# Optimization experiments

Hardware: AMD Instinct MI355X
Metric: run time of the kernel (lower is better)

The kernel has to match this reference:

```python
import jax, jax.numpy as jnp
import numpy as np

N = 10000    # nodes in batched graph
E = 160000   # edges (avg degree 16)
G = 64       # graphs in batch
F_IN = 128
H = 256      # hidden width (forced equal everywhere by fc_1(1024,..) and readout sums)
HEADS = 2


def setup_inputs() -> dict:
    ks = jax.random.split(jax.random.key(0), 24)
    def w(k, shape, fan_in):
        return jax.random.normal(k, shape, dtype=jnp.float32) * np.float32(1.0 / np.sqrt(fan_in))
    return {
        "h": jax.random.normal(ks[0], (N, F_IN), dtype=jnp.float32),
        "src": jax.random.randint(ks[1], (E,), 0, N, dtype=jnp.int32),
        "dst": jax.random.randint(ks[2], (E,), 0, N, dtype=jnp.int32),
        # sorted graph ids, every graph guaranteed non-empty (avoids -inf from MaxPooling)
        "graph_ids": ((jnp.arange(N) * G) // N).astype(jnp.int32),
        "gcn1_W": w(ks[3], (F_IN, H), F_IN), "gcn1_b": jnp.zeros((H,), jnp.float32),
        "gcn2_W": w(ks[4], (H, H), H),       "gcn2_b": jnp.zeros((H,), jnp.float32),
        "gcn3_W": w(ks[5], (H, H), H),       "gcn3_b": jnp.zeros((H,), jnp.float32),
        "gat1_W": w(ks[6], (F_IN, HEADS * H), F_IN),
        "gat1_al": w(ks[7], (HEADS, H), H), "gat1_ar": w(ks[8], (HEADS, H), H),
        "gat1_b": jnp.zeros((HEADS * H,), jnp.float32),
        "gat2_W": w(ks[9], (H, HEADS * H), H),
        "gat2_al": w(ks[10], (HEADS, H), H), "gat2_ar": w(ks[11], (HEADS, H), H),
        "gat2_b": jnp.zeros((HEADS * H,), jnp.float32),
        "gat3_W": w(ks[12], (H, HEADS * H), H),
        "gat3_al": w(ks[13], (HEADS, H), H), "gat3_ar": w(ks[14], (HEADS, H), H),
        "gat3_b": jnp.zeros((HEADS * H,), jnp.float32),
        "fc1_W": w(ks[15], (4 * H, 128), 4 * H), "fc1_b": jnp.zeros((128,), jnp.float32),
        "fc2_W": w(ks[16], (128, 2), 128),       "fc2_b": jnp.zeros((2,), jnp.float32),
    }


def _forward(h, src, dst, graph_ids,
             gcn1_W, gcn1_b, gcn2_W, gcn2_b, gcn3_W, gcn3_b,
             gat1_W, gat1_al, gat1_ar, gat1_b,
             gat2_W, gat2_al, gat2_ar, gat2_b,
             gat3_W, gat3_al, gat3_ar, gat3_b,
             fc1_W, fc1_b, fc2_W, fc2_b):
    ones_e = jnp.ones((E,), jnp.float32)
    # DGL GraphConv norm='both': D_out^{-1/2} on src side, D_in^{-1/2} on dst side (deg clamped to 1)
    d_src = jnp.clip(jax.ops.segment_sum(ones_e, src, num_segments=N), 1.0) ** -0.5
    d_dst = jnp.clip(jax.ops.segment_sum(ones_e, dst, num_segments=N), 1.0) ** -0.5
    counts = jnp.clip(jax.ops.segment_sum(jnp.ones((N,), jnp.float32), graph_ids, num_segments=G), 1.0)

    def gcn(x, W, b):
        agg = jax.ops.segment_sum((x * d_src[:, None])[src], dst, num_segments=N) * d_dst[:, None]
        return jax.nn.relu(agg @ W + b)

    def gat(x, W, al, ar, b):
        z = (x @ W).reshape(N, HEADS, H)                 # [N, heads, H]
        e = jax.nn.leaky_relu(jnp.sum(z * al, -1)[src] + jnp.sum(z * ar, -1)[dst], 0.2)  # [E, heads]
        ex = jnp.exp(e - jax.ops.segment_max(e, dst, num_segments=N)[dst])
        alpha = ex / jax.ops.segment_sum(ex, dst, num_segments=N)[dst]  # edge softmax per dst
        o = jax.ops.segment_sum(alpha[:, :, None] * z[src], dst, num_segments=N)  # [N, heads, H]
        return jax.nn.relu(o + b.reshape(1, HEADS, H)).mean(axis=1)     # mean over heads, as in source

    def avgp(x):
        return jax.ops.segment_sum(x, graph_ids, num_segments=G) / counts[:, None]
    def maxp(x):
        return jax.ops.segment_max(x, graph_ids, num_segments=G)
    def readout(x):
        return jnp.concatenate([avgp(x), maxp(x)], axis=1)

    gcn1 = gcn(h, gcn1_W, gcn1_b);   r1 = readout(gcn1)
    gcn2 = gcn(gcn1, gcn2_W, gcn2_b); r2 = readout(gcn2)
    gcn3 = gcn(gcn2, gcn3_W, gcn3_b); r3 = readout(gcn3)
    g1 = gat(h, gat1_W, gat1_al, gat1_ar, gat1_b)   # spat_read_out1 computed but unused (faithful)
    g2 = gat(g1, gat2_W, gat2_al, gat2_ar, gat2_b); s2 = readout(g2)
    g3 = gat(g2, gat3_W, gat3_al, gat3_ar, gat3_b)
    s3 = jnp.concatenate([avgp(g2), maxp(g3)], axis=1)  # source: avg(gat2), max(gat3)

    spec = r1 + r2 + r3
    spat = r1 + s2 + s3  # source bug preserved: spat_merged starts from spec_read_out1
    merged = jnp.concatenate([spec, spat], axis=1)       # [G, 1024]
    f1 = jax.nn.relu(merged @ fc1_W + fc1_b)             # dropout p=0.0 -> identity
    return jax.nn.sigmoid(f1 @ fc2_W + fc2_b)            # [G, 2]


def reference(h, src, dst, graph_ids,
              gcn1_W, gcn1_b, gcn2_W, gcn2_b, gcn3_W, gcn3_b,
              gat1_W, gat1_al, gat1_ar, gat1_b,
              gat2_W, gat2_al, gat2_ar, gat2_b,
              gat3_W, gat3_al, gat3_ar, gat3_b,
              fc1_W, fc1_b, fc2_W, fc2_b):
    return _forward(h, src, dst, graph_ids,
                    gcn1_W, gcn1_b, gcn2_W, gcn2_b, gcn3_W, gcn3_b,
                    gat1_W, gat1_al, gat1_ar, gat1_b,
                    gat2_W, gat2_al, gat2_ar, gat2_b,
                    gat3_W, gat3_al, gat3_ar, gat3_b,
                    fc1_W, fc1_b, fc2_W, fc2_b)
```

## Files before the change

kernel.cpp:

```cpp
#include <hip/hip_runtime.h>
#include <math.h>

#define NN 10000
#define EE 160000
#define GG 64
#define FIN 128
#define HH 256
#define ZW 512
#define RS 8
#define MAXDEG 128

typedef unsigned short u16;
using bf16x8 = __attribute__((ext_vector_type(8))) short;
using f32x4 = __attribute__((ext_vector_type(4))) float;

__device__ inline u16 f2bf(float x) {
  union { float f; unsigned u; } v; v.f = x;
  unsigned r = v.u + 0x7FFF + ((v.u >> 16) & 1);
  return (u16)(r >> 16);
}
__device__ inline float bf2f(u16 x) {
  union { unsigned u; float f; } v; v.u = ((unsigned)x) << 16; return v.f;
}
__device__ inline float bflo(unsigned pair) {
  union { unsigned u; float f; } v; v.u = pair << 16; return v.f;
}
__device__ inline float bfhi(unsigned pair) {
  union { unsigned u; float f; } v; v.u = pair & 0xFFFF0000u; return v.f;
}

#define BM 128
#define BN 64
#define BK 64
#define LPAD 8

struct SmemGemm { u16 As[BM][BK + LPAD]; u16 Bs[BN][BK + LPAD]; };
struct SmemGatGemm { u16 A[2][64][BK + LPAD]; u16 B[2][64][BK + LPAD]; };
struct SmemFuseV2 {
  float al[4][2][MAXDEG];
  int   idx[4][MAXDEG];
  float inv[4][2];
  float mm[4][2];
};


__global__ __launch_bounds__(256) void k_count_prep(
    const int* __restrict__ src, const int* __restrict__ dst, int* deg_src, int* deg_dst,
    const float* __restrict__ gcn1_W, u16* __restrict__ gcn1_Wt,
    const float* __restrict__ gcn2_W, u16* __restrict__ gcn2_Wt,
    const float* __restrict__ gcn3_W, u16* __restrict__ gcn3_Wt,
    const float* __restrict__ gat1_W, u16* __restrict__ gat1_Wt,
    const float* __restrict__ gat2_W, u16* __restrict__ gat2_Wt,
    const float* __restrict__ gat3_W, u16* __restrict__ gat3_Wt,
    const float* __restrict__ h, u16* __restrict__ h_bf,
    const float* __restrict__ al1, const float* __restrict__ ar1,
    const float* __restrict__ al2, const float* __restrict__ ar2,
    const float* __restrict__ al3, const float* __restrict__ ar3,
    float* __restrict__ wl1, float* __restrict__ wr1,
    float* __restrict__ wl2, float* __restrict__ wr2,
    float* __restrict__ wl3, float* __restrict__ wr3) {
  int bb = blockIdx.x, t = threadIdx.x;
  if (bb < 625) {
    int e = bb * 256 + t;
    if (e < EE) {
      atomicAdd(&deg_src[src[e]], 1);
      atomicAdd(&deg_dst[dst[e]], 1);
    }
    return;
  }
  int b = bb - 625;
  if (b < 1920) {
    const float* W; u16* Wt; int K, N, idx;
    if (b < 128)       { W = gcn1_W; Wt = gcn1_Wt; K = 128; N = 256; idx = b * 256 + t; }
    else if (b < 384)  { W = gcn2_W; Wt = gcn2_Wt; K = 256; N = 256; idx = (b - 128) * 256 + t; }
    else if (b < 640)  { W = gcn3_W; Wt = gcn3_Wt; K = 256; N = 256; idx = (b - 384) * 256 + t; }
    else if (b < 896)  { W = gat1_W; Wt = gat1_Wt; K = 128; N = 512; idx = (b - 640) * 256 + t; }
    else if (b < 1408) { W = gat2_W; Wt = gat2_Wt; K = 256; N = 512; idx = (b - 896) * 256 + t; }
    else               { W = gat3_W; Wt = gat3_Wt; K = 256; N = 512; idx = (b - 1408) * 256 + t; }
    int k = idx / N, n = idx - k * N;
    Wt[(size_t)n * K + k] = f2bf(W[idx]);
  } else if (b < 3170) {
    int idx = (b - 1920) * 256 + t;
    float4 v = *(const float4*)&h[(size_t)idx * 4];
    ushort4 o;
    o.x = f2bf(v.x); o.y = f2bf(v.y); o.z = f2bf(v.z); o.w = f2bf(v.w);
    *(ushort4*)&h_bf[(size_t)idx * 4] = o;
  } else {
    int jb = b - 3170;
    const float* W; const float* al; const float* ar; float* wl; float* wr; int K, i;
    if (jb == 0)      { W = gat1_W; al = al1; ar = ar1; wl = wl1; wr = wr1; K = 128; i = t; }
    else if (jb <= 2) { W = gat2_W; al = al2; ar = ar2; wl = wl2; wr = wr2; K = 256; i = (jb - 1) * 256 + t; }
    else              { W = gat3_W; al = al3; ar = ar3; wl = wl3; wr = wr3; K = 256; i = (jb - 3) * 256 + t; }
    int hh = i / K, k = i - hh * K;
    float sl = 0.f, sr = 0.f;
    for (int f = 0; f < HH; f++) {
      float wv = W[(size_t)k * ZW + hh * HH + f];
      sl += wv * al[hh * HH + f];
      sr += wv * ar[hh * HH + f];
    }
    wl[hh * K + k] = sl;
    wr[hh * K + k] = sr;
  }
}

__global__ __launch_bounds__(1024) void k_norms_scan(
    const int* __restrict__ deg_src, const int* __restrict__ deg_dst,
    const int* __restrict__ gid, float* dsrc, float* ddst, int* gstart, int* row_ptr) {
  if (blockIdx.x < 10) {
    int n = blockIdx.x * 1024 + threadIdx.x;
    if (n < NN) {
      int a = deg_src[n]; if (a < 1) a = 1;
      int b = deg_dst[n]; if (b < 1) b = 1;
      dsrc[n] = 1.0f / sqrtf((float)a);
      ddst[n] = 1.0f / sqrtf((float)b);
      if (n == 0) gstart[gid[0]] = 0;
      else if (gid[n] != gid[n - 1]) gstart[gid[n]] = n;
      if (n == NN - 1) gstart[GG] = NN;
    }
    return;
  }
  __shared__ int wsum[16];
  __shared__ int carry;
  int lane = threadIdx.x & 63, wid = threadIdx.x >> 6;
  if (threadIdx.x == 0) { carry = 0; row_ptr[0] = 0; }
  __syncthreads();
  for (int base = 0; base < NN; base += 1024) {
    int i = base + threadIdx.x;
    int x = (i < NN) ? deg_dst[i] : 0;
#pragma unroll
    for (int off = 1; off < 64; off <<= 1) {
      int t = __shfl_up(x, off);
      if (lane >= off) x += t;
    }
    if (lane == 63) wsum[wid] = x;
    __syncthreads();
    if (wid == 0 && lane < 16) {
      int y = wsum[lane];
#pragma unroll
      for (int off = 1; off < 16; off <<= 1) {
        int t = __shfl_up(y, off, 16);
        if (lane >= off) y += t;
      }
      wsum[lane] = y;
    }
    __syncthreads();
    int woff = (wid > 0) ? wsum[wid - 1] : 0;
    if (i < NN) row_ptr[i + 1] = carry + woff + x;
    int total = wsum[15];
    __syncthreads();
    if (threadIdx.x == 0) carry += total;
    __syncthreads();
  }
}

__global__ __launch_bounds__(64) void sort_rows_kernel(const int* __restrict__ row_ptr,
                                                       int* csr_src) {
  int n = blockIdx.x;
  int s0 = row_ptr[n];
  int L = row_ptr[n + 1] - s0;
  if (L <= 1) return;
  __shared__ int buf[512];
  if (L <= 512) {
    for (int i = threadIdx.x; i < L; i += 64) buf[i] = csr_src[s0 + i];
    __syncthreads();
    for (int i = threadIdx.x; i < L; i += 64) {
      int v = buf[i], r = 0;
      for (int j = 0; j < L; j++) {
        int u = buf[j];
        r += (u < v) || (u == v && j < i);
      }
      csr_src[s0 + r] = v;
    }
  } else if (threadIdx.x == 0) {
    for (int i = s0 + 1; i < s0 + L; i++) {
      int v = csr_src[i], j = i - 1;
      while (j >= s0 && csr_src[j] > v) { csr_src[j + 1] = csr_src[j]; j--; }
      csr_src[j + 1] = v;
    }
  }
}


__device__ inline void dev_gcn_agg(int n, int lane,
    const u16* __restrict__ xb, const float* __restrict__ dsrc, const float* __restrict__ ddst,
    const int* __restrict__ row_ptr, const int* __restrict__ csr_src,
    u16* __restrict__ out, int F) {
  int s0 = row_ptr[n], s1 = row_ptr[n + 1];
  float dd = ddst[n];
  if (F == 256) {
    int bf = lane * 4;
    float a0 = 0, a1 = 0, a2 = 0, a3 = 0;
    int e = s0;
    for (; e + 1 < s1; e += 2) {
      int sA = csr_src[e], sB = csr_src[e + 1];
      float wA = dsrc[sA], wB = dsrc[sB];
      uint2 vA = *(const uint2*)&xb[(size_t)sA * 256 + bf];
      uint2 vB = *(const uint2*)&xb[(size_t)sB * 256 + bf];
      a0 += wA * bflo(vA.x) + wB * bflo(vB.x);
      a1 += wA * bfhi(vA.x) + wB * bfhi(vB.x);
      a2 += wA * bflo(vA.y) + wB * bflo(vB.y);
      a3 += wA * bfhi(vA.y) + wB * bfhi(vB.y);
    }
    if (e < s1) {
      int s = csr_src[e];
      float w = dsrc[s];
      uint2 v = *(const uint2*)&xb[(size_t)s * 256 + bf];
      a0 += w * bflo(v.x); a1 += w * bfhi(v.x);
      a2 += w * bflo(v.y); a3 += w * bfhi(v.y);
    }
    ushort4 o;
    o.x = f2bf(a0 * dd); o.y = f2bf(a1 * dd); o.z = f2bf(a2 * dd); o.w = f2bf(a3 * dd);
    *(ushort4*)&out[(size_t)n * 256 + bf] = o;
  } else {
    int bf = lane * 2;
    float a0 = 0, a1 = 0;
    int e = s0;
    for (; e + 1 < s1; e += 2) {
      int sA = csr_src[e], sB = csr_src[e + 1];
      float wA = dsrc[sA], wB = dsrc[sB];
      unsigned vA = *(const unsigned*)&xb[(size_t)sA * 128 + bf];
      unsigned vB = *(const unsigned*)&xb[(size_t)sB * 128 + bf];
      a0 += wA * bflo(vA) + wB * bflo(vB);
      a1 += wA * bfhi(vA) + wB * bfhi(vB);
    }
    if (e < s1) {
      int s = csr_src[e];
      float w = dsrc[s];
      unsigned v = *(const unsigned*)&xb[(size_t)s * 128 + bf];
      a0 += w * bflo(v); a1 += w * bfhi(v);
    }
    ushort2 o;
    o.x = f2bf(a0 * dd); o.y = f2bf(a1 * dd);
    *(ushort2*)&out[(size_t)n * 128 + bf] = o;
  }
}

__device__ inline void dev_scores(int n, int lane, const float* __restrict__ x,
                                  const float* __restrict__ wl, const float* __restrict__ wr,
                                  float* __restrict__ asrc, float* __restrict__ adst, int K) {
  float a0 = 0, a1 = 0, b0 = 0, b1 = 0;
  for (int k = lane; k < K; k += 64) {
    float xv = x[(size_t)n * K + k];
    a0 += xv * wl[k];
    a1 += xv * wl[K + k];
    b0 += xv * wr[k];
    b1 += xv * wr[K + k];
  }
#pragma unroll
  for (int off = 32; off; off >>= 1) {
    a0 += __shfl_down(a0, off);
    a1 += __shfl_down(a1, off);
    b0 += __shfl_down(b0, off);
    b1 += __shfl_down(b1, off);
  }
  if (lane == 0) {
    asrc[n * 2 + 0] = a0; asrc[n * 2 + 1] = a1;
    adst[n * 2 + 0] = b0; adst[n * 2 + 1] = b1;
  }
}

__device__ inline void dev_scores_bf(int n, int lane, const u16* __restrict__ xb,
                                     const float* __restrict__ wl, const float* __restrict__ wr,
                                     float* __restrict__ asrc, float* __restrict__ adst) {
  float a0 = 0, a1 = 0, b0 = 0, b1 = 0;
#pragma unroll
  for (int idx = lane; idx < 128; idx += 64) {
    unsigned v = *(const unsigned*)&xb[(size_t)n * 256 + idx * 2];
    float lo = bflo(v), hi = bfhi(v);
    a0 += lo * wl[idx * 2] + hi * wl[idx * 2 + 1];
    a1 += lo * wl[256 + idx * 2] + hi * wl[256 + idx * 2 + 1];
    b0 += lo * wr[idx * 2] + hi * wr[idx * 2 + 1];
    b1 += lo * wr[256 + idx * 2] + hi * wr[256 + idx * 2 + 1];
  }
#pragma unroll
  for (int off = 32; off; off >>= 1) {
    a0 += __shfl_down(a0, off);
    a1 += __shfl_down(a1, off);
    b0 += __shfl_down(b0, off);
    b1 += __shfl_down(b1, off);
  }
  if (lane == 0) {
    asrc[n * 2 + 0] = a0; asrc[n * 2 + 1] = a1;
    adst[n * 2 + 0] = b0; adst[n * 2 + 1] = b1;
  }
}

template<int F>
__device__ inline void dev_gatfuse_v3(int n0, int tid,
    const u16* __restrict__ xb,
    const float* __restrict__ asrc, const float* __restrict__ adst,
    const int* __restrict__ row_ptr, const int* __restrict__ csr_src,
    u16* __restrict__ gx, SmemFuseV2& sf) {
  int w = tid >> 6, lane = tid & 63;
  {
    int n = n0 + w;
    int s0 = row_ptr[n];
    int deg = row_ptr[n + 1] - s0;
    float2 an = *(const float2*)&adst[n * 2];
    float m0 = -INFINITY, m1 = -INFINITY;
    if (deg <= MAXDEG) {
      for (int i = lane; i < deg; i += 64) {
        int s = csr_src[s0 + i];
        sf.idx[w][i] = s;
        float2 as = *(const float2*)&asrc[s * 2];
        float e0 = as.x + an.x; e0 = (e0 > 0.f) ? e0 : 0.2f * e0;
        float e1 = as.y + an.y; e1 = (e1 > 0.f) ? e1 : 0.2f * e1;
        sf.al[w][0][i] = e0; sf.al[w][1][i] = e1;
        m0 = fmaxf(m0, e0); m1 = fmaxf(m1, e1);
      }
#pragma unroll
      for (int off = 32; off; off >>= 1) {
        m0 = fmaxf(m0, __shfl_xor(m0, off));
        m1 = fmaxf(m1, __shfl_xor(m1, off));
      }
      float t0 = 0.f, t1 = 0.f;
      for (int i = lane; i < deg; i += 64) {
        float w0 = __expf(sf.al[w][0][i] - m0);
        float w1 = __expf(sf.al[w][1][i] - m1);
        sf.al[w][0][i] = w0; sf.al[w][1][i] = w1;
        t0 += w0; t1 += w1;
      }
#pragma unroll
      for (int off = 32; off; off >>= 1) {
        t0 += __shfl_xor(t0, off);
        t1 += __shfl_xor(t1, off);
      }
      if (lane == 0) {
        sf.inv[w][0] = (t0 > 0.f) ? 1.f / t0 : 0.f;
        sf.inv[w][1] = (t1 > 0.f) ? 1.f / t1 : 0.f;
      }
    } else {
      for (int i = lane; i < deg; i += 64) {
        float2 as = *(const float2*)&asrc[csr_src[s0 + i] * 2];
        float e0 = as.x + an.x; e0 = (e0 > 0.f) ? e0 : 0.2f * e0;
        float e1 = as.y + an.y; e1 = (e1 > 0.f) ? e1 : 0.2f * e1;
        m0 = fmaxf(m0, e0); m1 = fmaxf(m1, e1);
      }
#pragma unroll
      for (int off = 32; off; off >>= 1) {
        m0 = fmaxf(m0, __shfl_xor(m0, off));
        m1 = fmaxf(m1, __shfl_xor(m1, off));
      }
      float t0 = 0.f, t1 = 0.f;
      for (int i = lane; i < deg; i += 64) {
        float2 as = *(const float2*)&asrc[csr_src[s0 + i] * 2];
        float e0 = as.x + an.x; e0 = (e0 > 0.f) ? e0 : 0.2f * e0;
        float e1 = as.y + an.y; e1 = (e1 > 0.f) ? e1 : 0.2f * e1;
        t0 += __expf(e0 - m0); t1 += __expf(e1 - m1);
      }
#pragma unroll
      for (int off = 32; off; off >>= 1) {
        t0 += __shfl_xor(t0, off);
        t1 += __shfl_xor(t1, off);
      }
      if (lane == 0) {
        sf.inv[w][0] = (t0 > 0.f) ? 1.f / t0 : 0.f;
        sf.inv[w][1] = (t1 > 0.f) ? 1.f / t1 : 0.f;
        sf.mm[w][0] = m0; sf.mm[w][1] = m1;
      }
    }
  }
  __syncthreads();
  int slot = w;
  int p = lane;
  int n = n0 + slot;
  int s0 = row_ptr[n];
  int deg = row_ptr[n + 1] - s0;
  float i0 = sf.inv[slot][0], i1 = sf.inv[slot][1];
  if (F == 256) {
    float a0[4] = {0, 0, 0, 0}, a1[4] = {0, 0, 0, 0};
    if (deg <= MAXDEG) {
      int i = 0;
      for (; i + 1 < deg; i += 2) {
        int sA = sf.idx[slot][i], sB = sf.idx[slot][i + 1];
        float wA0 = sf.al[slot][0][i] * i0, wA1 = sf.al[slot][1][i] * i1;
        float wB0 = sf.al[slot][0][i + 1] * i0, wB1 = sf.al[slot][1][i + 1] * i1;
        uint2 vA = *(const uint2*)&xb[(size_t)sA * 256 + p * 4];
        uint2 vB = *(const uint2*)&xb[(size_t)sB * 256 + p * 4];
        float fA[4] = {bflo(vA.x), bfhi(vA.x), bflo(vA.y), bfhi(vA.y)};
        float fB[4] = {bflo(vB.x), bfhi(vB.x), bflo(vB.y), bfhi(vB.y)};
#pragma unroll
        for (int j = 0; j < 4; j++) {
          a0[j] += wA0 * fA[j] + wB0 * fB[j];
          a1[j] += wA1 * fA[j] + wB1 * fB[j];
        }
      }
      if (i < deg) {
        int s = sf.idx[slot][i];
        float w0 = sf.al[slot][0][i] * i0, w1 = sf.al[slot][1][i] * i1;
        uint2 v = *(const uint2*)&xb[(size_t)s * 256 + p * 4];
        float fv[4] = {bflo(v.x), bfhi(v.x), bflo(v.y), bfhi(v.y)};
#pragma unroll
        for (int j = 0; j < 4; j++) {
          a0[j] += w0 * fv[j];
          a1[j] += w1 * fv[j];
        }
      }
    } else {
      float mh0 = sf.mm[slot][0], mh1 = sf.mm[slot][1];
      float2 an = *(const float2*)&adst[n * 2];
      for (int i = 0; i < deg; i++) {
        int s = csr_src[s0 + i];
        float2 as = *(const float2*)&asrc[s * 2];
        float e0 = as.x + an.x; e0 = (e0 > 0.f) ? e0 : 0.2f * e0;
        float e1 = as.y + an.y; e1 = (e1 > 0.f) ? e1 : 0.2f * e1;
        float w0 = __expf(e0 - mh0) * i0, w1 = __expf(e1 - mh1) * i1;
        uint2 v = *(const uint2*)&xb[(size_t)s * 256 + p * 4];
        float fv[4] = {bflo(v.x), bfhi(v.x), bflo(v.y), bfhi(v.y)};
#pragma unroll
        for (int j = 0; j < 4; j++) {
          a0[j] += w0 * fv[j];
          a1[j] += w1 * fv[j];
        }
      }
    }
    ushort4 o0, o1;
    o0.x = f2bf(a0[0]); o0.y = f2bf(a0[1]); o0.z = f2bf(a0[2]); o0.w = f2bf(a0[3]);
    o1.x = f2bf(a1[0]); o1.y = f2bf(a1[1]); o1.z = f2bf(a1[2]); o1.w = f2bf(a1[3]);
    *(ushort4*)&gx[(size_t)n * 512 + p * 4] = o0;
    *(ushort4*)&gx[(size_t)n * 512 + 256 + p * 4] = o1;
  } else {
    float a00 = 0.f, a01 = 0.f, a10 = 0.f, a11 = 0.f;
    if (deg <= MAXDEG) {
      int i = 0;
      for (; i + 1 < deg; i += 2) {
        int sA = sf.idx[slot][i], sB = sf.idx[slot][i + 1];
        float wA0 = sf.al[slot][0][i] * i0, wA1 = sf.al[slot][1][i] * i1;
        float wB0 = sf.al[slot][0][i + 1] * i0, wB1 = sf.al[slot][1][i + 1] * i1;
        unsigned vA = *(const unsigned*)&xb[(size_t)sA * 128 + p * 2];
        unsigned vB = *(const unsigned*)&xb[(size_t)sB * 128 + p * 2];
        float lA = bflo(vA), hA = bfhi(vA), lB = bflo(vB), hB = bfhi(vB);
        a00 += wA0 * lA + wB0 * lB; a01 += wA0 * hA + wB0 * hB;
        a10 += wA1 * lA + wB1 * lB; a11 += wA1 * hA + wB1 * hB;
      }
      if (i < deg) {
        int s = sf.idx[slot][i];
        float w0 = sf.al[slot][0][i] * i0, w1 = sf.al[slot][1][i] * i1;
        unsigned v = *(const unsigned*)&xb[(size_t)s * 128 + p * 2];
        float lo = bflo(v), hi = bfhi(v);
        a00 += w0 * lo; a01 += w0 * hi;
        a10 += w1 * lo; a11 += w1 * hi;
      }
    } else {
      float mh0 = sf.mm[slot][0], mh1 = sf.mm[slot][1];
      float2 an = *(const float2*)&adst[n * 2];
      for (int i = 0; i < deg; i++) {
        int s = csr_src[s0 + i];
        float2 as = *(const float2*)&asrc[s * 2];
        float e0 = as.x + an.x; e0 = (e0 > 0.f) ? e0 : 0.2f * e0;
        float e1 = as.y + an.y; e1 = (e1 > 0.f) ? e1 : 0.2f * e1;
        float w0 = __expf(e0 - mh0) * i0, w1 = __expf(e1 - mh1) * i1;
        unsigned v = *(const unsigned*)&xb[(size_t)s * 128 + p * 2];
        float lo = bflo(v), hi = bfhi(v);
        a00 += w0 * lo; a01 += w0 * hi;
        a10 += w1 * lo; a11 += w1 * hi;
      }
    }
    ushort2 o0; o0.x = f2bf(a00); o0.y = f2bf(a01);
    ushort2 o1; o1.x = f2bf(a10); o1.y = f2bf(a11);
    *(ushort2*)&gx[(size_t)n * 256 + p * 2] = o0;
    *(ushort2*)&gx[(size_t)n * 256 + 128 + p * 2] = o1;
  }
}

__device__ inline void dev_gemm(const u16* __restrict__ A, const u16* __restrict__ Wt,
                                const float* __restrict__ bias, u16* __restrict__ Cb,
                                int K, int Nc, int relu, int bx, int by, int tid,
                                SmemGemm& sm) {
  int lane = tid & 63;
  int wid = tid >> 6;
  int wm = wid & 1, wn = wid >> 1;
  int l15 = lane & 15, lg = lane >> 4;
  int row0 = bx * BM;
  int col0 = by * BN;
  f32x4 acc[4][2] = {};
  for (int k0 = 0; k0 < K; k0 += BK) {
#pragma unroll
    for (int p = 0; p < 4; p++) {
      int c = p * 256 + tid;
      int r = c >> 3, k8 = c & 7;
      uint4 v = make_uint4(0, 0, 0, 0);
      int gr = row0 + r;
      if (gr < NN) v = *(const uint4*)&A[(size_t)gr * K + k0 + k8 * 8];
      *(uint4*)&sm.As[r][k8 * 8] = v;
    }
#pragma unroll
    for (int p = 0; p < 2; p++) {
      int c = p * 256 + tid;
      int r = c >> 3, k8 = c & 7;
      uint4 v = *(const uint4*)&Wt[(size_t)(col0 + r) * K + k0 + k8 * 8];
      *(uint4*)&sm.Bs[r][k8 * 8] = v;
    }
    __syncthreads();
#pragma unroll
    for (int ks = 0; ks < BK; ks += 32) {
      bf16x8 afr[4], bfr[2];
#pragma unroll
      for (int m = 0; m < 4; m++)
        afr[m] = *(const bf16x8*)&sm.As[wm * 64 + m * 16 + l15][ks + lg * 8];
#pragma unroll
      for (int nn = 0; nn < 2; nn++)
        bfr[nn] = *(const bf16x8*)&sm.Bs[wn * 32 + nn * 16 + l15][ks + lg * 8];
#pragma unroll
      for (int m = 0; m < 4; m++)
#pragma unroll
        for (int nn = 0; nn < 2; nn++)
          acc[m][nn] = __builtin_amdgcn_mfma_f32_16x16x32_bf16(afr[m], bfr[nn], acc[m][nn], 0, 0, 0);
    }
    __syncthreads();
  }
#pragma unroll
  for (int m = 0; m < 4; m++) {
#pragma unroll
    for (int nn = 0; nn < 2; nn++) {
      int gc = col0 + wn * 32 + nn * 16 + l15;
      float bv = bias ? bias[gc] : 0.f;
#pragma unroll
      for (int j = 0; j < 4; j++) {
        int gr = row0 + wm * 64 + m * 16 + lg * 4 + j;
        if (gr < NN) {
          float v = acc[m][nn][j] + bv;
          if (relu) v = fmaxf(v, 0.f);
          Cb[(size_t)gr * Nc + gc] = f2bf(v);
        }
      }
    }
  }
}

__device__ inline void dev_gat_gemm(const u16* __restrict__ gx, const u16* __restrict__ Wt,
                                    const float* __restrict__ bias, u16* __restrict__ gb,
                                    int K, int bx, int by, int tid, SmemGatGemm& sm) {
  int lane = tid & 63;
  int wid = tid >> 6;
  int wm = wid & 1, wn = wid >> 1;
  int l15 = lane & 15, lg = lane >> 4;
  int row0 = bx * 64;
  int col0 = by * 64;
  int str = 2 * K;
  f32x4 acc[2][2][2] = {};
  for (int k0 = 0; k0 < K; k0 += BK) {
#pragma unroll
    for (int hh = 0; hh < 2; hh++) {
#pragma unroll
      for (int p = 0; p < 2; p++) {
        int c = p * 256 + tid;
        int r = c >> 3, k8 = c & 7;
        int gr = row0 + r;
        uint4 v = make_uint4(0, 0, 0, 0);
        if (gr < NN) v = *(const uint4*)&gx[(size_t)gr * str + hh * K + k0 + k8 * 8];
        *(uint4*)&sm.A[hh][r][k8 * 8] = v;
      }
#pragma unroll
      for (int p = 0; p < 2; p++) {
        int c = p * 256 + tid;
        int r = c >> 3, k8 = c & 7;
        uint4 v = *(const uint4*)&Wt[(size_t)(hh * 256 + col0 + r) * K + k0 + k8 * 8];
        *(uint4*)&sm.B[hh][r][k8 * 8] = v;
      }
    }
    __syncthreads();
#pragma unroll
    for (int ks = 0; ks < BK; ks += 32) {
      bf16x8 af[2][2], bf_[2][2];
#pragma unroll
      for (int hh = 0; hh < 2; hh++) {
#pragma unroll
        for (int m = 0; m < 2; m++)
          af[hh][m] = *(const bf16x8*)&sm.A[hh][wm * 32 + m * 16 + l15][ks + lg * 8];
#pragma unroll
        for (int nn = 0; nn < 2; nn++)
          bf_[hh][nn] = *(const bf16x8*)&sm.B[hh][wn * 32 + nn * 16 + l15][ks + lg * 8];
      }
#pragma unroll
      for (int hh = 0; hh < 2; hh++)
#pragma unroll
        for (int m = 0; m < 2; m++)
#pragma unroll
          for (int nn = 0; nn < 2; nn++)
            acc[hh][m][nn] = __builtin_amdgcn_mfma_f32_16x16x32_bf16(af[hh][m], bf_[hh][nn], acc[hh][m][nn], 0, 0, 0);
    }
    __syncthreads();
  }
#pragma unroll
  for (int m = 0; m < 2; m++) {
#pragma unroll
    for (int nn = 0; nn < 2; nn++) {
      int gc = col0 + wn * 32 + nn * 16 + l15;
      float bv0 = bias[gc], bv1 = bias[256 + gc];
#pragma unroll
      for (int j = 0; j < 4; j++) {
        int gr = row0 + wm * 32 + m * 16 + lg * 4 + j;
        if (gr < NN) {
          float r0 = fmaxf(acc[0][m][nn][j] + bv0, 0.f);
          float r1 = fmaxf(acc[1][m][nn][j] + bv1, 0.f);
          gb[(size_t)gr * 256 + gc] = f2bf(0.5f * (r0 + r1));
        }
      }
    }
  }
}

__device__ inline void dev_stage1(const u16* __restrict__ x, int l, int g, int s, int f,
                                  const int* __restrict__ gstart, float* __restrict__ partial) {
  int n0 = gstart[g], n1 = gstart[g + 1];
  int cnt = n1 - n0;
  int chunk = (cnt + RS - 1) / RS;
  int a = n0 + s * chunk;
  int bnd = a + chunk; if (bnd > n1) bnd = n1;
  float sum = 0.f, mx = -INFINITY;
  for (int n = a; n < bnd; n++) {
    float v = bf2f(x[(size_t)n * HH + f]);
    sum += v;
    mx = fmaxf(mx, v);
  }
  size_t base = ((size_t)l * GG * RS + g * RS + s) * 2 * HH;
  partial[base + f] = sum;
  partial[base + HH + f] = mx;
}

__device__ inline float dev_stage2_val(const float* __restrict__ partial, int l, int g, int tt,
                                       const int* __restrict__ gstart) {
  int f = tt & 255, ismax = tt >> 8;
  size_t base = ((size_t)l * GG * RS + g * RS) * 2 * HH;
  if (!ismax) {
    float s = 0.f;
    for (int k = 0; k < RS; k++) s += partial[base + (size_t)k * 2 * HH + f];
    return s / (float)(gstart[g + 1] - gstart[g]);
  } else {
    float m = -INFINITY;
    for (int k = 0; k < RS; k++) m = fmaxf(m, partial[base + (size_t)k * 2 * HH + HH + f]);
    return m;
  }
}


__global__ __launch_bounds__(256) void k_fill_scores(
    const int* __restrict__ src, const int* __restrict__ dst,
    const int* __restrict__ row_ptr, int* fill, int* csr_src,
    const float* __restrict__ h, const float* __restrict__ wl1, const float* __restrict__ wr1,
    float* __restrict__ asrc, float* __restrict__ adst) {
  int b = blockIdx.x, t = threadIdx.x;
  if (b < 625) {
    int e = b * 256 + t;
    if (e < EE) {
      int d = dst[e];
      int p = atomicAdd(&fill[d], 1);
      csr_src[row_ptr[d] + p] = src[e];
    }
  } else {
    int n = (b - 625) * 4 + (t >> 6);
    if (n < NN) dev_scores(n, t & 63, h, wl1, wr1, asrc, adst, FIN);
  }
}

__global__ __launch_bounds__(256) void k_a1(
    const u16* __restrict__ h_bf, const float* __restrict__ dsrc, const float* __restrict__ ddst,
    const int* __restrict__ row_ptr, const int* __restrict__ csr_src,
    u16* __restrict__ zagg, const float* __restrict__ asrc, const float* __restrict__ adst,
    u16* __restrict__ gx) {
  __shared__ SmemFuseV2 sf;
  int b = blockIdx.x, t = threadIdx.x;
  if (b < 2500) {
    int n = b * 4 + (t >> 6);
    dev_gcn_agg(n, t & 63, h_bf, dsrc, ddst, row_ptr, csr_src, zagg, FIN);
  } else {
    dev_gatfuse_v3<128>((b - 2500) * 4, t, h_bf, asrc, adst, row_ptr, csr_src, gx, sf);
  }
}

__global__ __launch_bounds__(256) void k_b(
    const u16* __restrict__ zagg, const u16* __restrict__ gcn_Wt, const float* __restrict__ gcn_b,
    u16* __restrict__ ab_out, int Kg,
    const u16* __restrict__ gx, const u16* __restrict__ gat_Wt, const float* __restrict__ gat_b,
    u16* __restrict__ gb_out, int Ka) {
  __shared__ union { SmemGemm g; SmemGatGemm gg; } sm;
  int b = blockIdx.x, t = threadIdx.x;
  if (b < 316) {
    dev_gemm(zagg, gcn_Wt, gcn_b, ab_out, Kg, HH, 1, b % 79, b / 79, t, sm.g);
  } else {
    int i = b - 316;
    dev_gat_gemm(gx, gat_Wt, gat_b, gb_out, Ka, i / 4, i % 4, t, sm.gg);
  }
}

__global__ __launch_bounds__(256) void k_sc(
    const u16* __restrict__ gb_prev, const float* __restrict__ wl, const float* __restrict__ wr,
    float* __restrict__ asrc, float* __restrict__ adst) {
  int n = blockIdx.x * 4 + (threadIdx.x >> 6);
  dev_scores_bf(n, threadIdx.x & 63, gb_prev, wl, wr, asrc, adst);
}

__global__ __launch_bounds__(256) void k_af(
    const u16* __restrict__ ab_prev, const float* __restrict__ dsrc, const float* __restrict__ ddst,
    const int* __restrict__ row_ptr, const int* __restrict__ csr_src, u16* __restrict__ zagg,
    const u16* __restrict__ gb_prev, const float* __restrict__ asrc, const float* __restrict__ adst,
    u16* __restrict__ gx) {
  __shared__ SmemFuseV2 sf;
  int b = blockIdx.x, t = threadIdx.x;
  if (b < 2500) {
    int n = b * 4 + (t >> 6);
    dev_gcn_agg(n, t & 63, ab_prev, dsrc, ddst, row_ptr, csr_src, zagg, HH);
  } else {
    dev_gatfuse_v3<256>((b - 2500) * 4, t, gb_prev, asrc, adst, row_ptr, csr_src, gx, sf);
  }
}

struct Acts3 { const u16* a[3]; };
__global__ __launch_bounds__(256) void k_af3(
    const u16* __restrict__ ab_prev, const float* __restrict__ dsrc, const float* __restrict__ ddst,
    const int* __restrict__ row_ptr, const int* __restrict__ csr_src, u16* __restrict__ zagg,
    const u16* __restrict__ gb_prev, const float* __restrict__ asrc, const float* __restrict__ adst,
    u16* __restrict__ gx,
    Acts3 acts, const int* __restrict__ gstart, float* __restrict__ partial) {
  __shared__ SmemFuseV2 sf;
  int b = blockIdx.x, t = threadIdx.x;
  if (b < 2500) {
    int n = b * 4 + (t >> 6);
    dev_gcn_agg(n, t & 63, ab_prev, dsrc, ddst, row_ptr, csr_src, zagg, HH);
  } else if (b < 5000) {
    dev_gatfuse_v3<256>((b - 2500) * 4, t, gb_prev, asrc, adst, row_ptr, csr_src, gx, sf);
  } else {
    int i = b - 5000;
    int li = i >> 9, rem = i & 511;
    int lmap[3] = {0, 1, 3};
    dev_stage1(acts.a[li], lmap[li], rem >> 3, rem & 7, t, gstart, partial);
  }
}

__global__ __launch_bounds__(256) void k_r(
    const u16* __restrict__ ab3, const u16* __restrict__ gb3,
    const int* __restrict__ gstart, float* __restrict__ partial) {
  int b = blockIdx.x, t = threadIdx.x;
  const u16* x = (b < 512) ? ab3 : gb3;
  int l = (b < 512) ? 2 : 4;
  int i = b & 511;
  dev_stage1(x, l, i >> 3, i & 7, t, gstart, partial);
}

__global__ __launch_bounds__(512) void k_fc(
    const float* __restrict__ partial, const int* __restrict__ gstart,
    const float* __restrict__ W1, const float* __restrict__ b1,
    const float* __restrict__ W2, const float* __restrict__ b2, float* __restrict__ out) {
  int g = blockIdx.x;
  int t = threadIdx.x;
  __shared__ float row[1024];
  __shared__ float f1[128];
  {
    int c = t;
    float s0 = dev_stage2_val(partial, 0, g, c, gstart);
    float s1 = dev_stage2_val(partial, 1, g, c, gstart);
    float s2 = dev_stage2_val(partial, 2, g, c, gstart);
    float s3v = dev_stage2_val(partial, 3, g, c, gstart);
    float spec = s0 + s1 + s2;
    float last = (c < 256) ? s3v : dev_stage2_val(partial, 4, g, c, gstart);
    float spat = s0 + s3v + last;
    row[c] = spec;
    row[512 + c] = spat;
  }
  __syncthreads();
  if (t < 128) {
    float acc = b1[t];
    for (int k = 0; k < 1024; k++) acc += row[k] * W1[k * 128 + t];
    f1[t] = fmaxf(acc, 0.f);
  }
  __syncthreads();
  if (t < 2) {
    float a = b2[t];
    for (int k = 0; k < 128; k++) a += f1[k] * W2[k * 2 + t];
    out[g * 2 + t] = 1.f / (1.f + expf(-a));
  }
}

extern "C" void kernel_launch(void* const* d_in, const int* in_sizes, int n_in,
                              void* d_out, int out_size, void* d_ws, size_t ws_size,
                              hipStream_t stream) {
  const float* h      = (const float*)d_in[0];
  const int*   src    = (const int*)d_in[1];
  const int*   dst    = (const int*)d_in[2];
  const int*   gid    = (const int*)d_in[3];
  const float* gcn1_W = (const float*)d_in[4];  const float* gcn1_b = (const float*)d_in[5];
  const float* gcn2_W = (const float*)d_in[6];  const float* gcn2_b = (const float*)d_in[7];
  const float* gcn3_W = (const float*)d_in[8];  const float* gcn3_b = (const float*)d_in[9];
  const float* gat1_W = (const float*)d_in[10]; const float* gat1_al = (const float*)d_in[11];
  const float* gat1_ar= (const float*)d_in[12]; const float* gat1_b = (const float*)d_in[13];
  const float* gat2_W = (const float*)d_in[14]; const float* gat2_al = (const float*)d_in[15];
  const float* gat2_ar= (const float*)d_in[16]; const float* gat2_b = (const float*)d_in[17];
  const float* gat3_W = (const float*)d_in[18]; const float* gat3_al = (const float*)d_in[19];
  const float* gat3_ar= (const float*)d_in[20]; const float* gat3_b = (const float*)d_in[21];
  const float* fc1_W  = (const float*)d_in[22]; const float* fc1_b = (const float*)d_in[23];
  const float* fc2_W  = (const float*)d_in[24]; const float* fc2_b = (const float*)d_in[25];

  char* ws = (char*)d_ws;
  size_t off = 0;
  auto alloc = [&](size_t bytes) -> void* {
    void* p = ws + off;
    off += (bytes + 255) & ~(size_t)255;
    return p;
  };
  u16*   gx      = (u16*)alloc((size_t)NN * ZW * 2);
  u16*   Zagg    = (u16*)alloc((size_t)NN * HH * 2);
  u16*   h_bf    = (u16*)alloc((size_t)NN * FIN * 2);
  u16*   ab1     = (u16*)alloc((size_t)NN * HH * 2);
  u16*   ab2     = (u16*)alloc((size_t)NN * HH * 2);
  u16*   ab3     = (u16*)alloc((size_t)NN * HH * 2);
  u16*   gb1     = (u16*)alloc((size_t)NN * HH * 2);
  u16*   gb2     = (u16*)alloc((size_t)NN * HH * 2);
  u16*   gb3     = (u16*)alloc((size_t)NN * HH * 2);
  int*   row_ptr = (int*)alloc((NN + 1) * 4);
  int*   csr_src = (int*)alloc((size_t)EE * 4);
  int*   meta    = (int*)alloc((size_t)3 * NN * 4);
  int*   deg_src = meta;
  int*   deg_dst = meta + NN;
  int*   fill    = meta + 2 * NN;
  float* dsrc    = (float*)alloc(NN * 4);
  float* ddst    = (float*)alloc(NN * 4);
  int*   gstart  = (int*)alloc((GG + 1) * 4);
  float* asrc    = (float*)alloc(NN * 2 * 4);
  float* adst    = (float*)alloc(NN * 2 * 4);
  float* wl1     = (float*)alloc(2 * FIN * 4);
  float* wr1     = (float*)alloc(2 * FIN * 4);
  float* wl2     = (float*)alloc(2 * HH * 4);
  float* wr2     = (float*)alloc(2 * HH * 4);
  float* wl3     = (float*)alloc(2 * HH * 4);
  float* wr3     = (float*)alloc(2 * HH * 4);
  float* partial = (float*)alloc((size_t)5 * GG * RS * 2 * HH * 4);
  u16* gcn1_Wt = (u16*)alloc((size_t)FIN * HH * 2);
  u16* gcn2_Wt = (u16*)alloc((size_t)HH * HH * 2);
  u16* gcn3_Wt = (u16*)alloc((size_t)HH * HH * 2);
  u16* gat1_Wt = (u16*)alloc((size_t)FIN * ZW * 2);
  u16* gat2_Wt = (u16*)alloc((size_t)HH * ZW * 2);
  u16* gat3_Wt = (u16*)alloc((size_t)HH * ZW * 2);

  hipMemsetAsync(meta, 0, (size_t)3 * NN * 4, stream);
  k_count_prep<<<3800, 256, 0, stream>>>(
      src, dst, deg_src, deg_dst,
      gcn1_W, gcn1_Wt, gcn2_W, gcn2_Wt, gcn3_W, gcn3_Wt,
      gat1_W, gat1_Wt, gat2_W, gat2_Wt, gat3_W, gat3_Wt,
      h, h_bf,
      gat1_al, gat1_ar, gat2_al, gat2_ar, gat3_al, gat3_ar,
      wl1, wr1, wl2, wr2, wl3, wr3);
  k_norms_scan<<<11, 1024, 0, stream>>>(deg_src, deg_dst, gid, dsrc, ddst, gstart, row_ptr);
  k_fill_scores<<<3125, 256, 0, stream>>>(src, dst, row_ptr, fill, csr_src,
                                          h, wl1, wr1, asrc, adst);
  sort_rows_kernel<<<NN, 64, 0, stream>>>(row_ptr, csr_src);

  k_a1<<<5000, 256, 0, stream>>>(h_bf, dsrc, ddst, row_ptr, csr_src, Zagg, asrc, adst, gx);
  k_b<<<944, 256, 0, stream>>>(Zagg, gcn1_Wt, gcn1_b, ab1, FIN,
                               gx, gat1_Wt, gat1_b, gb1, FIN);
  k_sc<<<2500, 256, 0, stream>>>(gb1, wl2, wr2, asrc, adst);
  k_af<<<5000, 256, 0, stream>>>(ab1, dsrc, ddst, row_ptr, csr_src, Zagg,
                                 gb1, asrc, adst, gx);
  k_b<<<944, 256, 0, stream>>>(Zagg, gcn2_Wt, gcn2_b, ab2, HH,
                               gx, gat2_Wt, gat2_b, gb2, HH);
  k_sc<<<2500, 256, 0, stream>>>(gb2, wl3, wr3, asrc, adst);
  Acts3 acts; acts.a[0] = ab1; acts.a[1] = ab2; acts.a[2] = gb2;
  k_af3<<<6536, 256, 0, stream>>>(ab2, dsrc, ddst, row_ptr, csr_src, Zagg,
                                  gb2, asrc, adst, gx,
                                  acts, gstart, partial);
  k_b<<<944, 256, 0, stream>>>(Zagg, gcn3_Wt, gcn3_b, ab3, HH,
                               gx, gat3_Wt, gat3_b, gb3, HH);
  k_r<<<1024, 256, 0, stream>>>(ab3, gb3, gstart, partial);
  k_fc<<<GG, 512, 0, stream>>>(partial, gstart, fc1_W, fc1_b, fc2_W, fc2_b, (float*)d_out);
}
```

Before: 240.0 us.

## Fuse final-layer readout into FC kernel and single-pass degree scan

```diff
diff --git a/kernel.cpp b/kernel.cpp
--- a/kernel.cpp
+++ b/kernel.cpp
@@ -120,36 +120,42 @@
     return;
   }
   __shared__ int wsum[16];
-  __shared__ int carry;
-  int lane = threadIdx.x & 63, wid = threadIdx.x >> 6;
-  if (threadIdx.x == 0) { carry = 0; row_ptr[0] = 0; }
+  int t = threadIdx.x, lane = t & 63, wid = t >> 6;
+  int base = t * 10;
+  int loc[10];
+  int s = 0;
+#pragma unroll
+  for (int i = 0; i < 10; i++) {
+    int idx = base + i;
+    int v = (idx < NN) ? deg_dst[idx] : 0;
+    s += v;
+    loc[i] = s;
+  }
+  int x = s;
+#pragma unroll
+  for (int off = 1; off < 64; off <<= 1) {
+    int u = __shfl_up(x, off);
+    if (lane >= off) x += u;
+  }
+  if (lane == 63) wsum[wid] = x;
   __syncthreads();
-  for (int base = 0; base < NN; base += 1024) {
-    int i = base + threadIdx.x;
-    int x = (i < NN) ? deg_dst[i] : 0;
-#pragma unroll
-    for (int off = 1; off < 64; off <<= 1) {
-      int t = __shfl_up(x, off);
-      if (lane >= off) x += t;
-    }
-    if (lane == 63) wsum[wid] = x;
-    __syncthreads();
-    if (wid == 0 && lane < 16) {
-      int y = wsum[lane];
-#pragma unroll
-      for (int off = 1; off < 16; off <<= 1) {
-        int t = __shfl_up(y, off, 16);
-        if (lane >= off) y += t;
-      }
-      wsum[lane] = y;
-    }
-    __syncthreads();
-    int woff = (wid > 0) ? wsum[wid - 1] : 0;
-    if (i < NN) row_ptr[i + 1] = carry + woff + x;
-    int total = wsum[15];
-    __syncthreads();
-    if (threadIdx.x == 0) carry += total;
-    __syncthreads();
+  if (wid == 0 && lane < 16) {
+    int y = wsum[lane];
+#pragma unroll
+    for (int off = 1; off < 16; off <<= 1) {
+      int u = __shfl_up(y, off, 16);
+      if (lane >= off) y += u;
+    }
+    wsum[lane] = y;
+  }
+  __syncthreads();
+  int woff = (wid > 0) ? wsum[wid - 1] : 0;
+  int ex = woff + x - s;
+  if (t == 0) row_ptr[0] = 0;
+#pragma unroll
+  for (int i = 0; i < 10; i++) {
+    int idx = base + i;
+    if (idx < NN) row_ptr[idx + 1] = ex + loc[i];
   }
 }
 
@@ -728,32 +734,39 @@
   }
 }
 
-__global__ __launch_bounds__(256) void k_r(
-    const u16* __restrict__ ab3, const u16* __restrict__ gb3,
-    const int* __restrict__ gstart, float* __restrict__ partial) {
-  int b = blockIdx.x, t = threadIdx.x;
-  const u16* x = (b < 512) ? ab3 : gb3;
-  int l = (b < 512) ? 2 : 4;
-  int i = b & 511;
-  dev_stage1(x, l, i >> 3, i & 7, t, gstart, partial);
-}
-
 __global__ __launch_bounds__(512) void k_fc(
     const float* __restrict__ partial, const int* __restrict__ gstart,
+    const u16* __restrict__ ab3, const u16* __restrict__ gb3,
     const float* __restrict__ W1, const float* __restrict__ b1,
     const float* __restrict__ W2, const float* __restrict__ b2, float* __restrict__ out) {
   int g = blockIdx.x;
   int t = threadIdx.x;
   __shared__ float row[1024];
   __shared__ float f1[128];
+  __shared__ float r2s[512];
+  __shared__ float r4s[512];
+  {
+    const u16* arr = (t < 256) ? ab3 : gb3;
+    int f = t & 255;
+    int n0 = gstart[g], n1 = gstart[g + 1];
+    float sum = 0.f, mx = -INFINITY;
+    for (int n = n0; n < n1; n++) {
+      float v = bf2f(arr[(size_t)n * HH + f]);
+      sum += v;
+      mx = fmaxf(mx, v);
+    }
+    float avg = sum / (float)(n1 - n0);
+    if (t < 256) { r2s[f] = avg; r2s[256 + f] = mx; }
+    else         { r4s[f] = avg; r4s[256 + f] = mx; }
+  }
+  __syncthreads();
   {
     int c = t;
     float s0 = dev_stage2_val(partial, 0, g, c, gstart);
     float s1 = dev_stage2_val(partial, 1, g, c, gstart);
-    float s2 = dev_stage2_val(partial, 2, g, c, gstart);
     float s3v = dev_stage2_val(partial, 3, g, c, gstart);
-    float spec = s0 + s1 + s2;
-    float last = (c < 256) ? s3v : dev_stage2_val(partial, 4, g, c, gstart);
+    float spec = s0 + s1 + r2s[c];
+    float last = (c < 256) ? s3v : r4s[c];
     float spat = s0 + s3v + last;
     row[c] = spec;
     row[512 + c] = spat;
@@ -860,6 +873,6 @@
                                   acts, gstart, partial);
   k_b<<<944, 256, 0, stream>>>(Zagg, gcn3_Wt, gcn3_b, ab3, HH,
                                gx, gat3_Wt, gat3_b, gb3, HH);
-  k_r<<<1024, 256, 0, stream>>>(ab3, gb3, gstart, partial);
-  k_fc<<<GG, 512, 0, stream>>>(partial, gstart, fc1_W, fc1_b, fc2_W, fc2_b, (float*)d_out);
-}
+  k_fc<<<GG, 512, 0, stream>>>(partial, gstart, ab3, gb3,
+                               fc1_W, fc1_b, fc2_W, fc2_b, (float*)d_out);
+}
```

Result: slower. 264.8 us (+10.3%).
